# Optimization experiments

Measured on AMD Instinct MI355X. Metric: run time of the kernel, lower is better.

The kernel has to match this reference:

```python
import jax, jax.numpy as jnp
import numpy as np

N = 50000      # ncount
IN_CH = 256    # in_channels
OUT_CH = 128   # out_channels
NNZ = 800000   # nnz per sparse matrix (avg degree 16)


def _spmm(rows, cols, vals, dense, n_rows):
    # sparse(COO) @ dense : gather rows of dense by col index, scale, scatter-add by row
    contrib = vals[:, None] * dense[cols]              # [nnz, F]
    return jax.ops.segment_sum(contrib, rows, num_segments=n_rows)


def setup_inputs() -> dict:
    key = jax.random.key(0)
    ks = jax.random.split(key, 12)
    phi_indices = jnp.stack([
        jax.random.randint(ks[0], (NNZ,), 0, N),
        jax.random.randint(ks[1], (NNZ,), 0, N)])
    phi_values = jax.random.normal(ks[2], (NNZ,), dtype=jnp.float32)
    phi_inverse_indices = jnp.stack([
        jax.random.randint(ks[3], (NNZ,), 0, N),
        jax.random.randint(ks[4], (NNZ,), 0, N)])
    phi_inverse_values = jax.random.normal(ks[5], (NNZ,), dtype=jnp.float32)
    feature_indices = jnp.stack([
        jax.random.randint(ks[6], (NNZ,), 0, N),       # node index
        jax.random.randint(ks[7], (NNZ,), 0, IN_CH)])  # feature column
    feature_values = jax.random.normal(ks[8], (NNZ,), dtype=jnp.float32)
    # xavier_uniform for weight_matrix
    limit = float(np.sqrt(6.0 / (IN_CH + OUT_CH)))
    weight_matrix = jax.random.uniform(ks[9], (IN_CH, OUT_CH), jnp.float32, -limit, limit)
    # diagonal filter Theta init uniform(0.9, 1.1)
    diagonal_weight_filter = jax.random.uniform(ks[10], (N,), jnp.float32, 0.9, 1.1)
    return {
        "phi_indices": phi_indices,
        "phi_values": phi_values,
        "phi_inverse_indices": phi_inverse_indices,
        "phi_inverse_values": phi_inverse_values,
        "feature_indices": feature_indices,
        "feature_values": feature_values,
        "weight_matrix": weight_matrix,
        "diagonal_weight_filter": diagonal_weight_filter,
        "dropout": 0,
    }


def reference(phi_indices, phi_values, phi_inverse_indices, phi_inverse_values,
              feature_indices, feature_values, weight_matrix,
              diagonal_weight_filter, dropout):
    # rescaled_phi = phi @ diag(theta): scales column j of phi by theta[j]
    scaled_phi_vals = phi_values * diagonal_weight_filter[phi_indices[1]]
    # filtered = features(sparse N x IN) @ W  -> [N, OUT]
    filtered = _spmm(feature_indices[0], feature_indices[1], feature_values,
                     weight_matrix, N)
    # (phi * D * phi_inv) @ filtered computed associatively without dense N x N:
    tmp = _spmm(phi_inverse_indices[0], phi_inverse_indices[1],
                phi_inverse_values, filtered, N)              # phi_inv @ filtered
    localized = _spmm(phi_indices[0], phi_indices[1],
                      scaled_phi_vals, tmp, N)                # (phi D) @ tmp
    # dropout in eval mode (training=False) is identity
    return jax.nn.relu(localized)
```

## Files before the change

### kernel.cpp

```cpp
#include <hip/hip_runtime.h>
#include <hip/hip_fp16.h>


#define OUT_CH 128
#define HALF_CH 64
#define RPB 256
#define RPB_SHIFT 8
#define MAX_NB 256
#define EPB 4096
#define EPT 16
#define MAX_CHUNK 16
#define STAGE_CAP 8192


__global__ __launch_bounds__(256) void bucket_hist_kernel(
    const int* __restrict__ rows0, int n0,
    const int* __restrict__ rows1, int n1,
    const int* __restrict__ rows2, int n2,
    int* __restrict__ hist_part,
    int NB, int NBLK)
{
    int m = blockIdx.y;
    const int* rows = (m == 0) ? rows0 : (m == 1) ? rows1 : rows2;
    int nnz         = (m == 0) ? n0    : (m == 1) ? n1    : n2;
    __shared__ int bins[MAX_NB];
    if (threadIdx.x < NB) bins[threadIdx.x] = 0;
    __syncthreads();
    int base = blockIdx.x * EPB;
    #pragma unroll 4
    for (int k = 0; k < EPB / 256; ++k) {
        int i = base + k * 256 + threadIdx.x;
        if (i < nnz) atomicAdd(&bins[rows[i] >> RPB_SHIFT], 1);
    }
    __syncthreads();
    int* out = hist_part + ((size_t)(m * NBLK + blockIdx.x)) * NB;
    if (threadIdx.x < NB) out[threadIdx.x] = bins[threadIdx.x];
}


__global__ __launch_bounds__(256) void scan_blocks_wave_kernel(
    int* __restrict__ hist_part, int* __restrict__ totals, int NB, int NBLK)
{
    int w = blockIdx.x * 4 + (threadIdx.x >> 6);
    if (w >= 3 * NB) return;
    int lane = threadIdx.x & 63;
    int m = w / NB, b = w - m * NB;
    const int chunk = (NBLK + 63) >> 6;
    int base_blk = lane * chunk;

    int v[MAX_CHUNK];
    int sum = 0;
    for (int k = 0; k < chunk; ++k) {
        int blk = base_blk + k;
        int x = (blk < NBLK) ? hist_part[((size_t)(m * NBLK + blk)) * NB + b] : 0;
        v[k] = x; sum += x;
    }
    int incl = sum;
    #pragma unroll
    for (int s = 1; s < 64; s <<= 1) {
        int y = __shfl_up(incl, s);
        if (lane >= s) incl += y;
    }
    int run = incl - sum;
    for (int k = 0; k < chunk; ++k) {
        int blk = base_blk + k;
        if (blk < NBLK) {
            hist_part[((size_t)(m * NBLK + blk)) * NB + b] = run;
            run += v[k];
        }
    }
    if (lane == 63) totals[w] = incl;
}


__global__ __launch_bounds__(1024) void scan_buckets_kernel(
    const int* __restrict__ totals, int* __restrict__ bases, int NB)
{
    int m = blockIdx.x;
    int t = threadIdx.x;
    int x = (t < NB) ? totals[m * NB + t] : 0;
    int lane = t & 63, wid = t >> 6;
    int incl = x;
    #pragma unroll
    for (int s = 1; s < 64; s <<= 1) {
        int y = __shfl_up(incl, s);
        if (lane >= s) incl += y;
    }
    __shared__ int wtot[16];
    __shared__ int wbase[16];
    if (lane == 63) wtot[wid] = incl;
    __syncthreads();
    if (t == 0) {
        int run = 0;
        #pragma unroll
        for (int w = 0; w < 16; ++w) { int v = wtot[w]; wbase[w] = run; run += v; }
    }
    __syncthreads();
    if (t < NB) bases[m * NB + t] = wbase[wid] + incl - x;
}


__global__ __launch_bounds__(256) void bucket_scatter_kernel(
    const int* __restrict__ rows0, const int* __restrict__ cols0, const float* __restrict__ vals0, int n0,
    const int* __restrict__ rows1, const int* __restrict__ cols1, const float* __restrict__ vals1, int n1,
    const int* __restrict__ rows2, const int* __restrict__ cols2, const float* __restrict__ vals2, int n2,
    const float* __restrict__ theta,
    const int* __restrict__ hist_part, const int* __restrict__ bases,
    int2* __restrict__ eb0, int2* __restrict__ eb1, int2* __restrict__ eb2,
    int NB, int NBLK)
{
    int m = blockIdx.y;
    const int* rows; const int* cols; const float* vals; int nnz; int2* eb;
    if (m == 0)      { rows = rows0; cols = cols0; vals = vals0; nnz = n0; eb = eb0; }
    else if (m == 1) { rows = rows1; cols = cols1; vals = vals1; nnz = n1; eb = eb1; }
    else             { rows = rows2; cols = cols2; vals = vals2; nnz = n2; eb = eb2; }

    __shared__ int2 staged[EPB];
    __shared__ unsigned char bucket_of[EPB];
    __shared__ int lhist[MAX_NB];
    __shared__ int lstart[MAX_NB + 1];
    __shared__ int lcur[MAX_NB];
    __shared__ int gbase[MAX_NB];
    __shared__ int wtot[4], wbase[4];

    int t = threadIdx.x;
    if (t < NB) lhist[t] = 0;
    __syncthreads();

    int base = blockIdx.x * EPB;
    bool fold = (m == 2);

    int  bk[EPT];
    int2 pl[EPT];
    #pragma unroll
    for (int k = 0; k < EPT; ++k) {
        int i = base + k * 256 + t;
        if (i < nnz) {
            int r = rows[i], c = cols[i];
            float v = vals[i];
            if (fold) v *= theta[c];
            bk[k] = r >> RPB_SHIFT;
            pl[k] = make_int2(c | ((r & (RPB - 1)) << 16), __float_as_int(v));
            atomicAdd(&lhist[bk[k]], 1);
        } else bk[k] = -1;
    }
    __syncthreads();

    {
        int x = (t < NB) ? lhist[t] : 0;
        int lane = t & 63, wid = t >> 6;
        int incl = x;
        #pragma unroll
        for (int s = 1; s < 64; s <<= 1) {
            int y = __shfl_up(incl, s);
            if (lane >= s) incl += y;
        }
        if (lane == 63) wtot[wid] = incl;
        __syncthreads();
        if (t == 0) {
            int run = 0;
            #pragma unroll
            for (int w = 0; w < 4; ++w) { int v = wtot[w]; wbase[w] = run; run += v; }
            lstart[MAX_NB] = run;
        }
        __syncthreads();
        if (t < NB) {
            int excl = wbase[wid] + incl - x;
            lstart[t] = excl;
            lcur[t]   = excl;
            const int* hp = hist_part + ((size_t)(m * NBLK + blockIdx.x)) * NB;
            gbase[t] = bases[m * NB + t] + hp[t];
        }
    }
    __syncthreads();

    #pragma unroll
    for (int k = 0; k < EPT; ++k) {
        if (bk[k] >= 0) {
            int idx = atomicAdd(&lcur[bk[k]], 1);
            staged[idx] = pl[k];
            bucket_of[idx] = (unsigned char)bk[k];
        }
    }
    __syncthreads();

    int count = min(EPB, nnz - base);
    for (int i = t; i < count; i += 256) {
        int b = bucket_of[i];
        int dest = gbase[b] + (i - lstart[b]);
        eb[dest] = staged[i];
    }
}


__global__ __launch_bounds__(256) void bucket_to_csr_kernel(
    const int2* __restrict__ eb0, const int2* __restrict__ eb1, const int2* __restrict__ eb2,
    unsigned int* __restrict__ ec0, unsigned int* __restrict__ ec1, unsigned int* __restrict__ ec2,
    const int* __restrict__ bases,
    int* __restrict__ off,
    int n0, int n1, int n2, int NB, int n)
{
    int m = blockIdx.y;
    int b = blockIdx.x;
    const int2* eb; unsigned int* ec; int nnz;
    if (m == 0)      { eb = eb0; ec = ec0; nnz = n0; }
    else if (m == 1) { eb = eb1; ec = ec1; nnz = n1; }
    else             { eb = eb2; ec = ec2; nnz = n2; }
    int base = bases[m * NB + b];
    int end  = (b + 1 < NB) ? bases[m * NB + b + 1] : nnz;
    int cnt  = end - base;

    __shared__ unsigned int staged_c[STAGE_CAP];
    __shared__ int hist[RPB];
    __shared__ int cur[RPB];
    __shared__ int loc[RPB + 1];
    __shared__ int wtot[4];
    __shared__ int wbase[4];
    int t = threadIdx.x;
    hist[t] = 0; cur[t] = 0;
    __syncthreads();
    for (int i = base + t; i < end; i += 256)
        atomicAdd(&hist[(eb[i].x >> 16) & (RPB - 1)], 1);
    __syncthreads();
    {
        int x = hist[t];
        int lane = t & 63, wid = t >> 6;
        int incl = x;
        #pragma unroll
        for (int s = 1; s < 64; s <<= 1) {
            int y = __shfl_up(incl, s);
            if (lane >= s) incl += y;
        }
        if (lane == 63) wtot[wid] = incl;
        __syncthreads();
        if (t == 0) {
            int run = 0;
            #pragma unroll
            for (int w = 0; w < 4; ++w) { int v = wtot[w]; wbase[w] = run; run += v; }
        }
        __syncthreads();
        loc[t] = wbase[wid] + incl - x;
        if (t == RPB - 1) loc[RPB] = wbase[3] + incl;
    }
    __syncthreads();
    {
        int r = b * RPB + t;
        if (r <= n) off[(size_t)m * (n + 1) + r] = base + loc[t];
        if (b == NB - 1 && t == 0) off[(size_t)m * (n + 1) + n] = nnz;
    }
    if (cnt <= STAGE_CAP) {
        for (int i = base + t; i < end; i += 256) {
            int2 e = eb[i];
            int rl = (e.x >> 16) & (RPB - 1);
            int rk = atomicAdd(&cur[rl], 1);
            unsigned short h = __half_as_ushort(__float2half_rn(__int_as_float(e.y)));
            staged_c[loc[rl] + rk] = (unsigned int)(e.x & 0xFFFF) | ((unsigned int)h << 16);
        }
        __syncthreads();
        for (int i = t; i < cnt; i += 256)
            ec[base + i] = staged_c[i];
    } else {
        for (int i = base + t; i < end; i += 256) {
            int2 e = eb[i];
            int rl = (e.x >> 16) & (RPB - 1);
            int rk = atomicAdd(&cur[rl], 1);
            unsigned short h = __half_as_ushort(__float2half_rn(__int_as_float(e.y)));
            ec[base + loc[rl] + rk] = (unsigned int)(e.x & 0xFFFF) | ((unsigned int)h << 16);
        }
    }
}


template<bool SRC_H, bool DST_H, bool RELU>
__global__ __launch_bounds__(256) void spmm_csr_kernel(
    const int* __restrict__ off, const unsigned int* __restrict__ edges,
    const void* __restrict__ dense_v, void* __restrict__ out_v, int nrows)
{
    int lane = threadIdx.x & 63;
    int r = blockIdx.x * 4 + (threadIdx.x >> 6);
    if (r >= nrows) return;
    int j   = __builtin_amdgcn_readfirstlane(off[r]);
    int end = __builtin_amdgcn_readfirstlane(off[r + 1]);
    const float2*  df = (const float2*)dense_v;
    const __half2* dh = (const __half2*)dense_v;

    float2 a0 = make_float2(0.f, 0.f), a1 = make_float2(0.f, 0.f);

    for (; j + 8 <= end; j += 8) {
        unsigned int e[8]; float2 d[8];
        #pragma unroll
        for (int k = 0; k < 8; ++k) e[k] = edges[j + k];
        #pragma unroll
        for (int k = 0; k < 8; ++k) {
            if (SRC_H) d[k] = __half22float2(dh[(size_t)(e[k] & 0xFFFF) * HALF_CH + lane]);
            else       d[k] = df[(size_t)(e[k] & 0xFFFF) * HALF_CH + lane];
        }
        #pragma unroll
        for (int k = 0; k < 8; ++k) {
            float v = __half2float(__ushort_as_half((unsigned short)(e[k] >> 16)));
            if (k & 1) { a1.x = fmaf(v, d[k].x, a1.x); a1.y = fmaf(v, d[k].y, a1.y); }
            else       { a0.x = fmaf(v, d[k].x, a0.x); a0.y = fmaf(v, d[k].y, a0.y); }
        }
    }
    for (; j + 4 <= end; j += 4) {
        unsigned int e[4]; float2 d[4];
        #pragma unroll
        for (int k = 0; k < 4; ++k) e[k] = edges[j + k];
        #pragma unroll
        for (int k = 0; k < 4; ++k) {
            if (SRC_H) d[k] = __half22float2(dh[(size_t)(e[k] & 0xFFFF) * HALF_CH + lane]);
            else       d[k] = df[(size_t)(e[k] & 0xFFFF) * HALF_CH + lane];
        }
        #pragma unroll
        for (int k = 0; k < 4; ++k) {
            float v = __half2float(__ushort_as_half((unsigned short)(e[k] >> 16)));
            if (k & 1) { a1.x = fmaf(v, d[k].x, a1.x); a1.y = fmaf(v, d[k].y, a1.y); }
            else       { a0.x = fmaf(v, d[k].x, a0.x); a0.y = fmaf(v, d[k].y, a0.y); }
        }
    }
    for (; j < end; ++j) {
        unsigned int e0 = edges[j];
        float2 d0;
        if (SRC_H) d0 = __half22float2(dh[(size_t)(e0 & 0xFFFF) * HALF_CH + lane]);
        else       d0 = df[(size_t)(e0 & 0xFFFF) * HALF_CH + lane];
        float v0 = __half2float(__ushort_as_half((unsigned short)(e0 >> 16)));
        a0.x = fmaf(v0, d0.x, a0.x); a0.y = fmaf(v0, d0.y, a0.y);
    }
    float2 res = make_float2(a0.x + a1.x, a0.y + a1.y);
    if (RELU) { res.x = fmaxf(res.x, 0.f); res.y = fmaxf(res.y, 0.f); }
    if (DST_H) ((__half2*)out_v)[(size_t)r * HALF_CH + lane] = __float22half2_rn(res);
    else       ((float2*) out_v)[(size_t)r * HALF_CH + lane] = res;
}


__global__ __launch_bounds__(256) void spmm_atomic_kernel(
    const int* __restrict__ rows, const int* __restrict__ cols,
    const float* __restrict__ vals, const float* __restrict__ theta,
    const float* __restrict__ dense, float* __restrict__ out, int nnz)
{
    int idx = blockIdx.x * blockDim.x + threadIdx.x;
    int e = idx >> 7;
    int f = idx & (OUT_CH - 1);
    if (e >= nnz) return;
    int r = rows[e];
    int c = cols[e];
    float v = vals[e];
    if (theta != nullptr) v *= theta[c];
    atomicAdd(&out[(size_t)r * OUT_CH + f], v * dense[(size_t)c * OUT_CH + f]);
}

__global__ __launch_bounds__(256) void relu_kernel(float* __restrict__ out, int n4)
{
    int i = blockIdx.x * blockDim.x + threadIdx.x;
    if (i >= n4) return;
    float4 v = ((float4*)out)[i];
    v.x = fmaxf(v.x, 0.f); v.y = fmaxf(v.y, 0.f);
    v.z = fmaxf(v.z, 0.f); v.w = fmaxf(v.w, 0.f);
    ((float4*)out)[i] = v;
}


static inline size_t align16(size_t x) { return (x + 15) & ~(size_t)15; }

extern "C" void kernel_launch(void* const* d_in, const int* in_sizes, int n_in,
                              void* d_out, int out_size, void* d_ws, size_t ws_size,
                              hipStream_t stream)
{
    const int*   phi_idx   = (const int*)d_in[0];
    const float* phi_vals  = (const float*)d_in[1];
    const int*   phii_idx  = (const int*)d_in[2];
    const float* phii_vals = (const float*)d_in[3];
    const int*   feat_idx  = (const int*)d_in[4];
    const float* feat_vals = (const float*)d_in[5];
    const float* W         = (const float*)d_in[6];
    const float* theta     = (const float*)d_in[7];

    const int nnz_phi  = in_sizes[1];
    const int nnz_phii = in_sizes[3];
    const int nnz_feat = in_sizes[5];
    const int n_nodes  = in_sizes[7];
    const int in_ch    = in_sizes[6] / OUT_CH;
    const size_t dense_elems = (size_t)n_nodes * OUT_CH;
    const long long total_e = (long long)nnz_feat + nnz_phii + nnz_phi;

    const int NB = (n_nodes + RPB - 1) >> RPB_SHIFT;
    int max_nnz = nnz_feat > nnz_phii ? nnz_feat : nnz_phii;
    if (nnz_phi > max_nnz) max_nnz = nnz_phi;
    const int NBLK = (max_nnz + EPB - 1) / EPB;

    size_t p = 0;
    size_t filtered_off = p; p += align16(dense_elems * sizeof(__half));
    size_t tmp_off      = p; p += align16(dense_elems * sizeof(__half));
    size_t off_off      = p; p += align16((size_t)3 * (n_nodes + 1) * sizeof(int));
    size_t hp_off       = p; p += align16((size_t)3 * NBLK * NB * sizeof(int));
    size_t tot_off      = p; p += align16((size_t)3 * NB * sizeof(int));
    size_t bas_off      = p; p += align16((size_t)3 * NB * sizeof(int));
    size_t eb_off       = p; p += align16((size_t)total_e * sizeof(int2));
    size_t ec_off       = p; p += align16((size_t)total_e * sizeof(unsigned int));
    size_t need = p;

    char* ws = (char*)d_ws;
    dim3 block(256);

    bool fast_ok = (ws_size >= need) && (NB <= MAX_NB) && (n_nodes <= 65536) &&
                   (in_ch <= 65536) && (NBLK <= 64 * MAX_CHUNK);

    if (fast_ok) {
        __half* filtered = (__half*)(ws + filtered_off);
        __half* tmp      = (__half*)(ws + tmp_off);
        int* off_arr    = (int*)(ws + off_off);
        int* hist_part  = (int*)(ws + hp_off);
        int* totals     = (int*)(ws + tot_off);
        int* bases      = (int*)(ws + bas_off);
        int2* eb0 = (int2*)(ws + eb_off);
        int2* eb1 = eb0 + nnz_feat;
        int2* eb2 = eb1 + nnz_phii;
        unsigned int* ec0 = (unsigned int*)(ws + ec_off);
        unsigned int* ec1 = ec0 + nnz_feat;
        unsigned int* ec2 = ec1 + nnz_phii;

        const int* rows0 = feat_idx;  const int* cols0 = feat_idx + nnz_feat;
        const int* rows1 = phii_idx;  const int* cols1 = phii_idx + nnz_phii;
        const int* rows2 = phi_idx;   const int* cols2 = phi_idx  + nnz_phi;

        bucket_hist_kernel<<<dim3(NBLK, 3), block, 0, stream>>>(
            rows0, nnz_feat, rows1, nnz_phii, rows2, nnz_phi,
            hist_part, NB, NBLK);

        int nwaves = 3 * NB;
        scan_blocks_wave_kernel<<<dim3((nwaves + 3) / 4), block, 0, stream>>>(
            hist_part, totals, NB, NBLK);

        scan_buckets_kernel<<<dim3(3), dim3(1024), 0, stream>>>(totals, bases, NB);

        bucket_scatter_kernel<<<dim3(NBLK, 3), block, 0, stream>>>(
            rows0, cols0, feat_vals, nnz_feat,
            rows1, cols1, phii_vals, nnz_phii,
            rows2, cols2, phi_vals,  nnz_phi,
            theta, hist_part, bases, eb0, eb1, eb2, NB, NBLK);

        bucket_to_csr_kernel<<<dim3(NB, 3), block, 0, stream>>>(
            eb0, eb1, eb2, ec0, ec1, ec2, bases, off_arr,
            nnz_feat, nnz_phii, nnz_phi, NB, n_nodes);

        int* off_f  = off_arr;
        int* off_pi = off_arr + (n_nodes + 1);
        int* off_p  = off_arr + 2 * (n_nodes + 1);

        dim3 grid_r((unsigned)((n_nodes + 3) / 4));
        spmm_csr_kernel<false, true, false><<<grid_r, block, 0, stream>>>(
            off_f,  ec0, (const void*)W, (void*)filtered, n_nodes);
        spmm_csr_kernel<true, true, false><<<grid_r, block, 0, stream>>>(
            off_pi, ec1, (const void*)filtered, (void*)tmp, n_nodes);
        spmm_csr_kernel<true, false, true><<<grid_r, block, 0, stream>>>(
            off_p,  ec2, (const void*)tmp, d_out, n_nodes);
    } else {
        float* filtered = (float*)ws;
        float* tmp      = filtered + dense_elems;
        hipMemsetAsync(filtered, 0, 2 * dense_elems * sizeof(float), stream);
        hipMemsetAsync(d_out, 0, (size_t)out_size * sizeof(float), stream);
        {
            long long t = (long long)nnz_feat * OUT_CH;
            spmm_atomic_kernel<<<dim3((unsigned)((t + 255) / 256)), block, 0, stream>>>(
                feat_idx, feat_idx + nnz_feat, feat_vals, nullptr, W, filtered, nnz_feat);
        }
        {
            long long t = (long long)nnz_phii * OUT_CH;
            spmm_atomic_kernel<<<dim3((unsigned)((t + 255) / 256)), block, 0, stream>>>(
                phii_idx, phii_idx + nnz_phii, phii_vals, nullptr, filtered, tmp, nnz_phii);
        }
        {
            long long t = (long long)nnz_phi * OUT_CH;
            spmm_atomic_kernel<<<dim3((unsigned)((t + 255) / 256)), block, 0, stream>>>(
                phi_idx, phi_idx + nnz_phi, phi_vals, theta, tmp, (float*)d_out, nnz_phi);
        }
        {
            int n4 = out_size / 4;
            relu_kernel<<<dim3((n4 + 255) / 256), block, 0, stream>>>((float*)d_out, n4);
        }
    }
}
```

Before: 218.1 us.

## Replace two-level bucket sort CSR build with global atomic row counting sort

Replaces the bucket histogram, block scan, bucket scatter and per-bucket CSR sort with a simpler counting sort. Per-row counts come from global atomics, two small scan kernels produce the row offsets, and a scatter uses global atomic cursors to place packed col/half-value entries directly. This removes the intermediate int2 bucket buffer and one full pass over the edges. In exchange it relies on heavy global atomic traffic and random writes, and the order of entries within a row becomes nondeterministic, which can change floating-point summation order.

```diff
diff --git a/kernel.cpp b/kernel.cpp
--- a/kernel.cpp
+++ b/kernel.cpp
@@ -9,76 +9,41 @@
 #define MAX_NB 256
 #define EPB 4096
 #define EPT 16
-#define MAX_CHUNK 16
-#define STAGE_CAP 8192
-
-
-__global__ __launch_bounds__(256) void bucket_hist_kernel(
+
+
+__global__ __launch_bounds__(256) void zero4_kernel(int4* __restrict__ p, int n4)
+{
+    int i = blockIdx.x * 256 + threadIdx.x;
+    if (i < n4) p[i] = make_int4(0, 0, 0, 0);
+}
+
+
+__global__ __launch_bounds__(256) void row_hist_kernel(
     const int* __restrict__ rows0, int n0,
     const int* __restrict__ rows1, int n1,
     const int* __restrict__ rows2, int n2,
-    int* __restrict__ hist_part,
-    int NB, int NBLK)
+    int* __restrict__ cnt, int S)
 {
     int m = blockIdx.y;
     const int* rows = (m == 0) ? rows0 : (m == 1) ? rows1 : rows2;
     int nnz         = (m == 0) ? n0    : (m == 1) ? n1    : n2;
-    __shared__ int bins[MAX_NB];
-    if (threadIdx.x < NB) bins[threadIdx.x] = 0;
-    __syncthreads();
+    int* c = cnt + (size_t)m * S;
     int base = blockIdx.x * EPB;
-    #pragma unroll 4
-    for (int k = 0; k < EPB / 256; ++k) {
+    #pragma unroll
+    for (int k = 0; k < EPT; ++k) {
         int i = base + k * 256 + threadIdx.x;
-        if (i < nnz) atomicAdd(&bins[rows[i] >> RPB_SHIFT], 1);
-    }
-    __syncthreads();
-    int* out = hist_part + ((size_t)(m * NBLK + blockIdx.x)) * NB;
-    if (threadIdx.x < NB) out[threadIdx.x] = bins[threadIdx.x];
-}
-
-
-__global__ __launch_bounds__(256) void scan_blocks_wave_kernel(
-    int* __restrict__ hist_part, int* __restrict__ totals, int NB, int NBLK)
-{
-    int w = blockIdx.x * 4 + (threadIdx.x >> 6);
-    if (w >= 3 * NB) return;
-    int lane = threadIdx.x & 63;
-    int m = w / NB, b = w - m * NB;
-    const int chunk = (NBLK + 63) >> 6;
-    int base_blk = lane * chunk;
-
-    int v[MAX_CHUNK];
-    int sum = 0;
-    for (int k = 0; k < chunk; ++k) {
-        int blk = base_blk + k;
-        int x = (blk < NBLK) ? hist_part[((size_t)(m * NBLK + blk)) * NB + b] : 0;
-        v[k] = x; sum += x;
-    }
-    int incl = sum;
-    #pragma unroll
-    for (int s = 1; s < 64; s <<= 1) {
-        int y = __shfl_up(incl, s);
-        if (lane >= s) incl += y;
-    }
-    int run = incl - sum;
-    for (int k = 0; k < chunk; ++k) {
-        int blk = base_blk + k;
-        if (blk < NBLK) {
-            hist_part[((size_t)(m * NBLK + blk)) * NB + b] = run;
-            run += v[k];
-        }
-    }
-    if (lane == 63) totals[w] = incl;
-}
-
-
-__global__ __launch_bounds__(1024) void scan_buckets_kernel(
-    const int* __restrict__ totals, int* __restrict__ bases, int NB)
-{
-    int m = blockIdx.x;
-    int t = threadIdx.x;
-    int x = (t < NB) ? totals[m * NB + t] : 0;
+        if (i < nnz) atomicAdd(&c[rows[i]], 1);
+    }
+}
+
+
+__global__ __launch_bounds__(256) void scan_chunks_kernel(
+    const int* __restrict__ cnt, int* __restrict__ off,
+    int* __restrict__ totals, int S, int n, int NB)
+{
+    int m = blockIdx.y, b = blockIdx.x, t = threadIdx.x;
+    int r = b * RPB + t;
+    int x = cnt[(size_t)m * S + r];
     int lane = t & 63, wid = t >> 6;
     int incl = x;
     #pragma unroll
@@ -86,186 +51,78 @@
         int y = __shfl_up(incl, s);
         if (lane >= s) incl += y;
     }
-    __shared__ int wtot[16];
-    __shared__ int wbase[16];
+    __shared__ int wtot[4], wbase[4];
     if (lane == 63) wtot[wid] = incl;
     __syncthreads();
     if (t == 0) {
         int run = 0;
         #pragma unroll
-        for (int w = 0; w < 16; ++w) { int v = wtot[w]; wbase[w] = run; run += v; }
+        for (int w = 0; w < 4; ++w) { int v = wtot[w]; wbase[w] = run; run += v; }
+        totals[m * NB + b] = run;
     }
     __syncthreads();
-    if (t < NB) bases[m * NB + t] = wbase[wid] + incl - x;
-}
-
-
-__global__ __launch_bounds__(256) void bucket_scatter_kernel(
+    int excl = wbase[wid] + incl - x;
+    if (r < n) off[(size_t)m * (n + 1) + r] = excl;
+}
+
+
+__global__ __launch_bounds__(256) void offcur_kernel(
+    const int* __restrict__ totals, int* __restrict__ off,
+    int* __restrict__ cnt, int S, int n, int NB,
+    int n0, int n1, int n2)
+{
+    int m = blockIdx.y, b = blockIdx.x, t = threadIdx.x;
+    int x = (t < b) ? totals[m * NB + t] : 0;
+    int lane = t & 63, wid = t >> 6;
+    int v = x;
+    #pragma unroll
+    for (int s = 1; s < 64; s <<= 1) v += __shfl_xor(v, s);
+    __shared__ int ws[4];
+    __shared__ int base_s;
+    if (lane == 0) ws[wid] = v;
+    __syncthreads();
+    if (t == 0) base_s = ws[0] + ws[1] + ws[2] + ws[3];
+    __syncthreads();
+    int base = base_s;
+    int r = b * RPB + t;
+    if (r < n) {
+        int val = off[(size_t)m * (n + 1) + r] + base;
+        off[(size_t)m * (n + 1) + r] = val;
+        cnt[(size_t)m * S + r] = val;
+    }
+    if (b == NB - 1 && t == 0) {
+        int nnz = (m == 0) ? n0 : (m == 1) ? n1 : n2;
+        off[(size_t)m * (n + 1) + n] = nnz;
+    }
+}
+
+
+__global__ __launch_bounds__(256) void scatter_csr_kernel(
     const int* __restrict__ rows0, const int* __restrict__ cols0, const float* __restrict__ vals0, int n0,
     const int* __restrict__ rows1, const int* __restrict__ cols1, const float* __restrict__ vals1, int n1,
     const int* __restrict__ rows2, const int* __restrict__ cols2, const float* __restrict__ vals2, int n2,
     const float* __restrict__ theta,
-    const int* __restrict__ hist_part, const int* __restrict__ bases,
-    int2* __restrict__ eb0, int2* __restrict__ eb1, int2* __restrict__ eb2,
-    int NB, int NBLK)
+    int* __restrict__ cur, int S,
+    unsigned int* __restrict__ ec0, unsigned int* __restrict__ ec1, unsigned int* __restrict__ ec2)
 {
     int m = blockIdx.y;
-    const int* rows; const int* cols; const float* vals; int nnz; int2* eb;
-    if (m == 0)      { rows = rows0; cols = cols0; vals = vals0; nnz = n0; eb = eb0; }
-    else if (m == 1) { rows = rows1; cols = cols1; vals = vals1; nnz = n1; eb = eb1; }
-    else             { rows = rows2; cols = cols2; vals = vals2; nnz = n2; eb = eb2; }
-
-    __shared__ int2 staged[EPB];
-    __shared__ unsigned char bucket_of[EPB];
-    __shared__ int lhist[MAX_NB];
-    __shared__ int lstart[MAX_NB + 1];
-    __shared__ int lcur[MAX_NB];
-    __shared__ int gbase[MAX_NB];
-    __shared__ int wtot[4], wbase[4];
-
-    int t = threadIdx.x;
-    if (t < NB) lhist[t] = 0;
-    __syncthreads();
-
+    const int* rows; const int* cols; const float* vals; int nnz; unsigned int* ec;
+    if (m == 0)      { rows = rows0; cols = cols0; vals = vals0; nnz = n0; ec = ec0; }
+    else if (m == 1) { rows = rows1; cols = cols1; vals = vals1; nnz = n1; ec = ec1; }
+    else             { rows = rows2; cols = cols2; vals = vals2; nnz = n2; ec = ec2; }
+    int* c = cur + (size_t)m * S;
+    bool fold = (m == 2);
     int base = blockIdx.x * EPB;
-    bool fold = (m == 2);
-
-    int  bk[EPT];
-    int2 pl[EPT];
     #pragma unroll
     for (int k = 0; k < EPT; ++k) {
-        int i = base + k * 256 + t;
+        int i = base + k * 256 + threadIdx.x;
         if (i < nnz) {
-            int r = rows[i], c = cols[i];
+            int r = rows[i], col = cols[i];
             float v = vals[i];
-            if (fold) v *= theta[c];
-            bk[k] = r >> RPB_SHIFT;
-            pl[k] = make_int2(c | ((r & (RPB - 1)) << 16), __float_as_int(v));
-            atomicAdd(&lhist[bk[k]], 1);
-        } else bk[k] = -1;
-    }
-    __syncthreads();
-
-    {
-        int x = (t < NB) ? lhist[t] : 0;
-        int lane = t & 63, wid = t >> 6;
-        int incl = x;
-        #pragma unroll
-        for (int s = 1; s < 64; s <<= 1) {
-            int y = __shfl_up(incl, s);
-            if (lane >= s) incl += y;
-        }
-        if (lane == 63) wtot[wid] = incl;
-        __syncthreads();
-        if (t == 0) {
-            int run = 0;
-            #pragma unroll
-            for (int w = 0; w < 4; ++w) { int v = wtot[w]; wbase[w] = run; run += v; }
-            lstart[MAX_NB] = run;
-        }
-        __syncthreads();
-        if (t < NB) {
-            int excl = wbase[wid] + incl - x;
-            lstart[t] = excl;
-            lcur[t]   = excl;
-            const int* hp = hist_part + ((size_t)(m * NBLK + blockIdx.x)) * NB;
-            gbase[t] = bases[m * NB + t] + hp[t];
-        }
-    }
-    __syncthreads();
-
-    #pragma unroll
-    for (int k = 0; k < EPT; ++k) {
-        if (bk[k] >= 0) {
-            int idx = atomicAdd(&lcur[bk[k]], 1);
-            staged[idx] = pl[k];
-            bucket_of[idx] = (unsigned char)bk[k];
-        }
-    }
-    __syncthreads();
-
-    int count = min(EPB, nnz - base);
-    for (int i = t; i < count; i += 256) {
-        int b = bucket_of[i];
-        int dest = gbase[b] + (i - lstart[b]);
-        eb[dest] = staged[i];
-    }
-}
-
-
-__global__ __launch_bounds__(256) void bucket_to_csr_kernel(
-    const int2* __restrict__ eb0, const int2* __restrict__ eb1, const int2* __restrict__ eb2,
-    unsigned int* __restrict__ ec0, unsigned int* __restrict__ ec1, unsigned int* __restrict__ ec2,
-    const int* __restrict__ bases,
-    int* __restrict__ off,
-    int n0, int n1, int n2, int NB, int n)
-{
-    int m = blockIdx.y;
-    int b = blockIdx.x;
-    const int2* eb; unsigned int* ec; int nnz;
-    if (m == 0)      { eb = eb0; ec = ec0; nnz = n0; }
-    else if (m == 1) { eb = eb1; ec = ec1; nnz = n1; }
-    else             { eb = eb2; ec = ec2; nnz = n2; }
-    int base = bases[m * NB + b];
-    int end  = (b + 1 < NB) ? bases[m * NB + b + 1] : nnz;
-    int cnt  = end - base;
-
-    __shared__ unsigned int staged_c[STAGE_CAP];
-    __shared__ int hist[RPB];
-    __shared__ int cur[RPB];
-    __shared__ int loc[RPB + 1];
-    __shared__ int wtot[4];
-    __shared__ int wbase[4];
-    int t = threadIdx.x;
-    hist[t] = 0; cur[t] = 0;
-    __syncthreads();
-    for (int i = base + t; i < end; i += 256)
-        atomicAdd(&hist[(eb[i].x >> 16) & (RPB - 1)], 1);
-    __syncthreads();
-    {
-        int x = hist[t];
-        int lane = t & 63, wid = t >> 6;
-        int incl = x;
-        #pragma unroll
-        for (int s = 1; s < 64; s <<= 1) {
-            int y = __shfl_up(incl, s);
-            if (lane >= s) incl += y;
-        }
-        if (lane == 63) wtot[wid] = incl;
-        __syncthreads();
-        if (t == 0) {
-            int run = 0;
-            #pragma unroll
-            for (int w = 0; w < 4; ++w) { int v = wtot[w]; wbase[w] = run; run += v; }
-        }
-        __syncthreads();
-        loc[t] = wbase[wid] + incl - x;
-        if (t == RPB - 1) loc[RPB] = wbase[3] + incl;
-    }
-    __syncthreads();
-    {
-        int r = b * RPB + t;
-        if (r <= n) off[(size_t)m * (n + 1) + r] = base + loc[t];
-        if (b == NB - 1 && t == 0) off[(size_t)m * (n + 1) + n] = nnz;
-    }
-    if (cnt <= STAGE_CAP) {
-        for (int i = base + t; i < end; i += 256) {
-            int2 e = eb[i];
-            int rl = (e.x >> 16) & (RPB - 1);
-            int rk = atomicAdd(&cur[rl], 1);
-            unsigned short h = __half_as_ushort(__float2half_rn(__int_as_float(e.y)));
-            staged_c[loc[rl] + rk] = (unsigned int)(e.x & 0xFFFF) | ((unsigned int)h << 16);
-        }
-        __syncthreads();
-        for (int i = t; i < cnt; i += 256)
-            ec[base + i] = staged_c[i];
-    } else {
-        for (int i = base + t; i < end; i += 256) {
-            int2 e = eb[i];
-            int rl = (e.x >> 16) & (RPB - 1);
-            int rk = atomicAdd(&cur[rl], 1);
-            unsigned short h = __half_as_ushort(__float2half_rn(__int_as_float(e.y)));
-            ec[base + loc[rl] + rk] = (unsigned int)(e.x & 0xFFFF) | ((unsigned int)h << 16);
+            if (fold) v *= theta[col];
+            int pos = atomicAdd(&c[r], 1);
+            unsigned short h = __half_as_ushort(__float2half_rn(v));
+            ec[pos] = (unsigned int)(col & 0xFFFF) | ((unsigned int)h << 16);
         }
     }
 }
@@ -384,6 +241,7 @@
     const long long total_e = (long long)nnz_feat + nnz_phii + nnz_phi;
 
     const int NB = (n_nodes + RPB - 1) >> RPB_SHIFT;
+    const int S  = NB * RPB;
     int max_nnz = nnz_feat > nnz_phii ? nnz_feat : nnz_phii;
     if (nnz_phi > max_nnz) max_nnz = nnz_phi;
     const int NBLK = (max_nnz + EPB - 1) / EPB;
@@ -392,10 +250,8 @@
     size_t filtered_off = p; p += align16(dense_elems * sizeof(__half));
     size_t tmp_off      = p; p += align16(dense_elems * sizeof(__half));
     size_t off_off      = p; p += align16((size_t)3 * (n_nodes + 1) * sizeof(int));
-    size_t hp_off       = p; p += align16((size_t)3 * NBLK * NB * sizeof(int));
+    size_t cnt_off      = p; p += align16((size_t)3 * S * sizeof(int));
     size_t tot_off      = p; p += align16((size_t)3 * NB * sizeof(int));
-    size_t bas_off      = p; p += align16((size_t)3 * NB * sizeof(int));
-    size_t eb_off       = p; p += align16((size_t)total_e * sizeof(int2));
     size_t ec_off       = p; p += align16((size_t)total_e * sizeof(unsigned int));
     size_t need = p;
 
@@ -403,18 +259,14 @@
     dim3 block(256);
 
     bool fast_ok = (ws_size >= need) && (NB <= MAX_NB) && (n_nodes <= 65536) &&
-                   (in_ch <= 65536) && (NBLK <= 64 * MAX_CHUNK);
+                   (in_ch <= 65536);
 
     if (fast_ok) {
         __half* filtered = (__half*)(ws + filtered_off);
         __half* tmp      = (__half*)(ws + tmp_off);
         int* off_arr    = (int*)(ws + off_off);
-        int* hist_part  = (int*)(ws + hp_off);
+        int* cnt        = (int*)(ws + cnt_off);
         int* totals     = (int*)(ws + tot_off);
-        int* bases      = (int*)(ws + bas_off);
-        int2* eb0 = (int2*)(ws + eb_off);
-        int2* eb1 = eb0 + nnz_feat;
-        int2* eb2 = eb1 + nnz_phii;
         unsigned int* ec0 = (unsigned int*)(ws + ec_off);
         unsigned int* ec1 = ec0 + nnz_feat;
         unsigned int* ec2 = ec1 + nnz_phii;
@@ -423,25 +275,27 @@
         const int* rows1 = phii_idx;  const int* cols1 = phii_idx + nnz_phii;
         const int* rows2 = phi_idx;   const int* cols2 = phi_idx  + nnz_phi;
 
-        bucket_hist_kernel<<<dim3(NBLK, 3), block, 0, stream>>>(
-            rows0, nnz_feat, rows1, nnz_phii, rows2, nnz_phi,
-            hist_part, NB, NBLK);
-
-        int nwaves = 3 * NB;
-        scan_blocks_wave_kernel<<<dim3((nwaves + 3) / 4), block, 0, stream>>>(
-            hist_part, totals, NB, NBLK);
-
-        scan_buckets_kernel<<<dim3(3), dim3(1024), 0, stream>>>(totals, bases, NB);
-
-        bucket_scatter_kernel<<<dim3(NBLK, 3), block, 0, stream>>>(
+        {
+            int n4 = (3 * S) / 4;
+            zero4_kernel<<<dim3((n4 + 255) / 256), block, 0, stream>>>(
+                (int4*)cnt, n4);
+        }
+
+        row_hist_kernel<<<dim3(NBLK, 3), block, 0, stream>>>(
+            rows0, nnz_feat, rows1, nnz_phii, rows2, nnz_phi, cnt, S);
+
+        scan_chunks_kernel<<<dim3(NB, 3), block, 0, stream>>>(
+            cnt, off_arr, totals, S, n_nodes, NB);
+
+        offcur_kernel<<<dim3(NB, 3), block, 0, stream>>>(
+            totals, off_arr, cnt, S, n_nodes, NB,
+            nnz_feat, nnz_phii, nnz_phi);
+
+        scatter_csr_kernel<<<dim3(NBLK, 3), block, 0, stream>>>(
             rows0, cols0, feat_vals, nnz_feat,
             rows1, cols1, phii_vals, nnz_phii,
             rows2, cols2, phi_vals,  nnz_phi,
-            theta, hist_part, bases, eb0, eb1, eb2, NB, NBLK);
-
-        bucket_to_csr_kernel<<<dim3(NB, 3), block, 0, stream>>>(
-            eb0, eb1, eb2, ec0, ec1, ec2, bases, off_arr,
-            nnz_feat, nnz_phii, nnz_phi, NB, n_nodes);
+            theta, cnt, S, ec0, ec1, ec2);
 
         int* off_f  = off_arr;
         int* off_pi = off_arr + (n_nodes + 1);
```

New measurement: 458.4 us. +110.2%, slower.

## Merge scan kernels and allocate bucket slots via atomic cursors; unroll SpMM gather by 16

Applied to the files above, without the earlier changes.

The two-kernel per-block prefix scan is replaced by a single small kernel that sums each bucket's per-block counts and writes bucket bases plus a cursor array. The scatter kernel now takes its global slot with an atomicAdd on the cursor and reuses the precomputed per-block histogram instead of rebuilding it with shared atomics. This removes a kernel launch and redundant histogram work, but the order of edges within a bucket becomes nondeterministic across blocks, and the scan now walks all blocks serially per bucket. Separately, the CSR SpMM gets a 16-edge unrolled loop to keep more gathers in flight, at the cost of more registers.

```diff
diff --git a/kernel.cpp b/kernel.cpp
--- a/kernel.cpp
+++ b/kernel.cpp
@@ -9,7 +9,6 @@
 #define MAX_NB 256
 #define EPB 4096
 #define EPT 16
-#define MAX_CHUNK 16
 #define STAGE_CAP 8192
 
 
@@ -38,65 +37,37 @@
 }
 
 
-__global__ __launch_bounds__(256) void scan_blocks_wave_kernel(
-    int* __restrict__ hist_part, int* __restrict__ totals, int NB, int NBLK)
-{
-    int w = blockIdx.x * 4 + (threadIdx.x >> 6);
-    if (w >= 3 * NB) return;
-    int lane = threadIdx.x & 63;
-    int m = w / NB, b = w - m * NB;
-    const int chunk = (NBLK + 63) >> 6;
-    int base_blk = lane * chunk;
-
-    int v[MAX_CHUNK];
+__global__ __launch_bounds__(256) void scan_cursors_kernel(
+    const int* __restrict__ hist_part,
+    int* __restrict__ bases, int* __restrict__ cursor, int NB, int NBLK)
+{
+    int m = blockIdx.x, t = threadIdx.x;
     int sum = 0;
-    for (int k = 0; k < chunk; ++k) {
-        int blk = base_blk + k;
-        int x = (blk < NBLK) ? hist_part[((size_t)(m * NBLK + blk)) * NB + b] : 0;
-        v[k] = x; sum += x;
-    }
+    if (t < NB) {
+        const int* hp = hist_part + (size_t)m * NBLK * NB + t;
+        for (int blk = 0; blk < NBLK; ++blk) sum += hp[(size_t)blk * NB];
+    }
+    int lane = t & 63, wid = t >> 6;
     int incl = sum;
     #pragma unroll
     for (int s = 1; s < 64; s <<= 1) {
         int y = __shfl_up(incl, s);
         if (lane >= s) incl += y;
     }
-    int run = incl - sum;
-    for (int k = 0; k < chunk; ++k) {
-        int blk = base_blk + k;
-        if (blk < NBLK) {
-            hist_part[((size_t)(m * NBLK + blk)) * NB + b] = run;
-            run += v[k];
-        }
-    }
-    if (lane == 63) totals[w] = incl;
-}
-
-
-__global__ __launch_bounds__(1024) void scan_buckets_kernel(
-    const int* __restrict__ totals, int* __restrict__ bases, int NB)
-{
-    int m = blockIdx.x;
-    int t = threadIdx.x;
-    int x = (t < NB) ? totals[m * NB + t] : 0;
-    int lane = t & 63, wid = t >> 6;
-    int incl = x;
-    #pragma unroll
-    for (int s = 1; s < 64; s <<= 1) {
-        int y = __shfl_up(incl, s);
-        if (lane >= s) incl += y;
-    }
-    __shared__ int wtot[16];
-    __shared__ int wbase[16];
+    __shared__ int wtot[4], wbase[4];
     if (lane == 63) wtot[wid] = incl;
     __syncthreads();
     if (t == 0) {
         int run = 0;
         #pragma unroll
-        for (int w = 0; w < 16; ++w) { int v = wtot[w]; wbase[w] = run; run += v; }
-    }
-    __syncthreads();
-    if (t < NB) bases[m * NB + t] = wbase[wid] + incl - x;
+        for (int w = 0; w < 4; ++w) { int v = wtot[w]; wbase[w] = run; run += v; }
+    }
+    __syncthreads();
+    if (t < NB) {
+        int excl = wbase[wid] + incl - sum;
+        bases[m * NB + t] = excl;
+        cursor[m * NB + t] = excl;
+    }
 }
 
 
@@ -105,7 +76,7 @@
     const int* __restrict__ rows1, const int* __restrict__ cols1, const float* __restrict__ vals1, int n1,
     const int* __restrict__ rows2, const int* __restrict__ cols2, const float* __restrict__ vals2, int n2,
     const float* __restrict__ theta,
-    const int* __restrict__ hist_part, const int* __restrict__ bases,
+    const int* __restrict__ hist_part, int* __restrict__ cursor,
     int2* __restrict__ eb0, int2* __restrict__ eb1, int2* __restrict__ eb2,
     int NB, int NBLK)
 {
@@ -117,16 +88,12 @@
 
     __shared__ int2 staged[EPB];
     __shared__ unsigned char bucket_of[EPB];
-    __shared__ int lhist[MAX_NB];
-    __shared__ int lstart[MAX_NB + 1];
+    __shared__ int lstart[MAX_NB];
     __shared__ int lcur[MAX_NB];
     __shared__ int gbase[MAX_NB];
     __shared__ int wtot[4], wbase[4];
 
     int t = threadIdx.x;
-    if (t < NB) lhist[t] = 0;
-    __syncthreads();
-
     int base = blockIdx.x * EPB;
     bool fold = (m == 2);
 
@@ -141,15 +108,14 @@
             if (fold) v *= theta[c];
             bk[k] = r >> RPB_SHIFT;
             pl[k] = make_int2(c | ((r & (RPB - 1)) << 16), __float_as_int(v));
-            atomicAdd(&lhist[bk[k]], 1);
         } else bk[k] = -1;
     }
-    __syncthreads();
 
     {
-        int x = (t < NB) ? lhist[t] : 0;
+        const int* hp = hist_part + ((size_t)(m * NBLK + blockIdx.x)) * NB;
+        int lh = (t < NB) ? hp[t] : 0;
         int lane = t & 63, wid = t >> 6;
-        int incl = x;
+        int incl = lh;
         #pragma unroll
         for (int s = 1; s < 64; s <<= 1) {
             int y = __shfl_up(incl, s);
@@ -161,15 +127,13 @@
             int run = 0;
             #pragma unroll
             for (int w = 0; w < 4; ++w) { int v = wtot[w]; wbase[w] = run; run += v; }
-            lstart[MAX_NB] = run;
         }
         __syncthreads();
         if (t < NB) {
-            int excl = wbase[wid] + incl - x;
+            int excl = wbase[wid] + incl - lh;
             lstart[t] = excl;
             lcur[t]   = excl;
-            const int* hp = hist_part + ((size_t)(m * NBLK + blockIdx.x)) * NB;
-            gbase[t] = bases[m * NB + t] + hp[t];
+            gbase[t] = atomicAdd(&cursor[m * NB + t], lh);
         }
     }
     __syncthreads();
@@ -286,6 +250,22 @@
 
     float2 a0 = make_float2(0.f, 0.f), a1 = make_float2(0.f, 0.f);
 
+    for (; j + 16 <= end; j += 16) {
+        unsigned int e[16]; float2 d[16];
+        #pragma unroll
+        for (int k = 0; k < 16; ++k) e[k] = edges[j + k];
+        #pragma unroll
+        for (int k = 0; k < 16; ++k) {
+            if (SRC_H) d[k] = __half22float2(dh[(size_t)(e[k] & 0xFFFF) * HALF_CH + lane]);
+            else       d[k] = df[(size_t)(e[k] & 0xFFFF) * HALF_CH + lane];
+        }
+        #pragma unroll
+        for (int k = 0; k < 16; ++k) {
+            float v = __half2float(__ushort_as_half((unsigned short)(e[k] >> 16)));
+            if (k & 1) { a1.x = fmaf(v, d[k].x, a1.x); a1.y = fmaf(v, d[k].y, a1.y); }
+            else       { a0.x = fmaf(v, d[k].x, a0.x); a0.y = fmaf(v, d[k].y, a0.y); }
+        }
+    }
     for (; j + 8 <= end; j += 8) {
         unsigned int e[8]; float2 d[8];
         #pragma unroll
@@ -393,8 +373,8 @@
     size_t tmp_off      = p; p += align16(dense_elems * sizeof(__half));
     size_t off_off      = p; p += align16((size_t)3 * (n_nodes + 1) * sizeof(int));
     size_t hp_off       = p; p += align16((size_t)3 * NBLK * NB * sizeof(int));
-    size_t tot_off      = p; p += align16((size_t)3 * NB * sizeof(int));
     size_t bas_off      = p; p += align16((size_t)3 * NB * sizeof(int));
+    size_t cur_off      = p; p += align16((size_t)3 * NB * sizeof(int));
     size_t eb_off       = p; p += align16((size_t)total_e * sizeof(int2));
     size_t ec_off       = p; p += align16((size_t)total_e * sizeof(unsigned int));
     size_t need = p;
@@ -403,15 +383,15 @@
     dim3 block(256);
 
     bool fast_ok = (ws_size >= need) && (NB <= MAX_NB) && (n_nodes <= 65536) &&
-                   (in_ch <= 65536) && (NBLK <= 64 * MAX_CHUNK);
+                   (in_ch <= 65536);
 
     if (fast_ok) {
         __half* filtered = (__half*)(ws + filtered_off);
         __half* tmp      = (__half*)(ws + tmp_off);
         int* off_arr    = (int*)(ws + off_off);
         int* hist_part  = (int*)(ws + hp_off);
-        int* totals     = (int*)(ws + tot_off);
         int* bases      = (int*)(ws + bas_off);
+        int* cursor     = (int*)(ws + cur_off);
         int2* eb0 = (int2*)(ws + eb_off);
         int2* eb1 = eb0 + nnz_feat;
         int2* eb2 = eb1 + nnz_phii;
@@ -427,17 +407,14 @@
             rows0, nnz_feat, rows1, nnz_phii, rows2, nnz_phi,
             hist_part, NB, NBLK);
 
-        int nwaves = 3 * NB;
-        scan_blocks_wave_kernel<<<dim3((nwaves + 3) / 4), block, 0, stream>>>(
-            hist_part, totals, NB, NBLK);
-
-        scan_buckets_kernel<<<dim3(3), dim3(1024), 0, stream>>>(totals, bases, NB);
+        scan_cursors_kernel<<<dim3(3), block, 0, stream>>>(
+            hist_part, bases, cursor, NB, NBLK);
 
         bucket_scatter_kernel<<<dim3(NBLK, 3), block, 0, stream>>>(
             rows0, cols0, feat_vals, nnz_feat,
             rows1, cols1, phii_vals, nnz_phii,
             rows2, cols2, phi_vals,  nnz_phi,
-            theta, hist_part, bases, eb0, eb1, eb2, NB, NBLK);
+            theta, hist_part, cursor, eb0, eb1, eb2, NB, NBLK);
 
         bucket_to_csr_kernel<<<dim3(NB, 3), block, 0, stream>>>(
             eb0, eb1, eb2, ec0, ec1, ec2, bases, off_arr,
```

Result: slower. 261.8 us (+20.1%).
